# Performance work log

Hardware: AMD Instinct MI355X
Metric: run time of the kernel (lower is better)

The kernel has to match this reference:

```python
import jax, jax.numpy as jnp
import numpy as np


def setup_inputs() -> dict:
    key = jax.random.key(0)
    ks = jax.random.split(key, 6)
    B, N, D, E, S, H = 4, 4096, 768, 4, 1024, 3072
    sc = lambda d: 1.0 / np.sqrt(d)
    return {
        "x": jax.random.normal(ks[0], (B, N, D), dtype=jnp.float32),
        "phi": jax.random.normal(ks[1], (E, S, D), dtype=jnp.float32) * sc(D),
        "w1": jax.random.normal(ks[2], (E, D, H), dtype=jnp.float32) * sc(D),
        "b1": jnp.zeros((E, H), dtype=jnp.float32),
        "w2": jax.random.normal(ks[3], (E, H, D), dtype=jnp.float32) * sc(H),
        "b2": jnp.zeros((E, D), dtype=jnp.float32),
    }


def reference(x, phi, w1, b1, w2, b2):
    # x: [B,N,D], phi: [E,S,D]
    logits = jnp.einsum('bnd,esd->bnes', x, phi)          # [B,N,E,S]
    B, N, E, S = logits.shape
    dispatch = jax.nn.softmax(logits, axis=1)             # softmax over tokens
    combine = jax.nn.softmax(
        logits.reshape(B, N, E * S), axis=-1
    ).reshape(B, N, E, S)                                 # softmax over all slots
    slots = jnp.einsum('bnd,bnes->besd', x, dispatch)     # [B,E,S,D]
    h = jax.nn.gelu(jnp.einsum('besd,edh->besh', slots, w1) + b1[None, :, None, :])
    y = jnp.einsum('besh,ehd->besd', h, w2) + b2[None, :, None, :]
    out = jnp.einsum('besd,bnes->bnd', y, combine)        # [B,N,D]
    return out
```

## Files before the change

kernel.cpp:

```cpp
#include <hip/hip_runtime.h>
#include <hip/hip_bf16.h>

using u16 = unsigned short;
using short8 = __attribute__((ext_vector_type(8))) short;
using floatx4 = __attribute__((ext_vector_type(4))) float;

#define DEVI static __device__ __forceinline__

constexpr int cB = 4, cN = 4096, cD = 768, cE = 4, cS = 1024, cH = 3072;
constexpr int cES = cE * cS;

DEVI u16 f2bf(float f) {
  union { float f; unsigned u; } v; v.f = f;
  unsigned r = v.u + 0x7fffu + ((v.u >> 16) & 1u);
  return (u16)(r >> 16);
}
DEVI float bf2f(u16 b) {
  union { unsigned u; float f; } v; v.u = ((unsigned)b) << 16;
  return v.f;
}
DEVI float gelu_tanh(float x) {
  float z = 1.5957691216057308f * (x + 0.044715f * x * x * x);
  z = fminf(fmaxf(z, -30.f), 30.f);
  float e = __expf(z);
  float t = (e - 1.f) / (e + 1.f);
  return 0.5f * x * (1.f + t);
}

DEVI void glds16(const u16* g, u16* l) {
  __builtin_amdgcn_global_load_lds(
      (const __attribute__((address_space(1))) void*)g,
      (__attribute__((address_space(3))) void*)l, 16, 0, 0);
}

__global__ __launch_bounds__(256) void zero_kernel(float* __restrict__ p, int n) {
  int i = blockIdx.x * 256 + threadIdx.x;
  if (i < n) p[i] = 0.f;
}

__global__ __launch_bounds__(256) void convert_kernel(const float* __restrict__ in,
                                                      u16* __restrict__ out, long n) {
  long stride = (long)gridDim.x * 256 * 4;
  for (long idx = ((long)blockIdx.x * 256 + threadIdx.x) * 4; idx < n; idx += stride) {
    float4 v = *(const float4*)(in + idx);
    ushort4 o;
    o.x = f2bf(v.x); o.y = f2bf(v.y); o.z = f2bf(v.z); o.w = f2bf(v.w);
    *(ushort4*)(out + idx) = o;
  }
}

template <typename Tin>
__global__ __launch_bounds__(256) void transpose_bf16_kernel(const Tin* __restrict__ in,
                                                             u16* __restrict__ out,
                                                             int R, int C,
                                                             long strideIn, long strideOut) {
  __shared__ u16 tile[64][66];
  const Tin* inb = in + (long)blockIdx.z * strideIn;
  u16* outb = out + (long)blockIdx.z * strideOut;
  const int r0 = blockIdx.y * 64, c0 = blockIdx.x * 64;
  const int tid = threadIdx.x;
#pragma unroll
  for (int i = 0; i < 4; i++) {
    int v = i * 256 + tid;
    int r = v >> 4, c4 = (v & 15) * 4;
    if constexpr (sizeof(Tin) == 4) {
      float4 f = *(const float4*)&inb[(long)(r0 + r) * C + (c0 + c4)];
      tile[r][c4 + 0] = f2bf(f.x); tile[r][c4 + 1] = f2bf(f.y);
      tile[r][c4 + 2] = f2bf(f.z); tile[r][c4 + 3] = f2bf(f.w);
    } else {
      ushort4 u = *(const ushort4*)&inb[(long)(r0 + r) * C + (c0 + c4)];
      tile[r][c4 + 0] = u.x; tile[r][c4 + 1] = u.y;
      tile[r][c4 + 2] = u.z; tile[r][c4 + 3] = u.w;
    }
  }
  __syncthreads();
#pragma unroll
  for (int i = 0; i < 4; i++) {
    int w = i * 256 + tid;
    int orow = w >> 4, oc4 = (w & 15) * 4;
    ushort4 u;
    u.x = tile[oc4 + 0][orow]; u.y = tile[oc4 + 1][orow];
    u.z = tile[oc4 + 2][orow]; u.w = tile[oc4 + 3][orow];
    *(ushort4*)&outb[(long)(c0 + orow) * R + (r0 + oc4)] = u;
  }
}

template <int EPI>
__global__ __launch_bounds__(256, 2) void gemm_nt(const u16* __restrict__ A,
                                                  const u16* __restrict__ Bm,
                                                  void* __restrict__ Cout,
                                                  int M, int Nn, int K,
                                                  long ldA, long ldB, long ldC,
                                                  long strideA, long strideB, int modB,
                                                  long strideC,
                                                  const float* __restrict__ epiVec,
                                                  long epiStride, int epiMod) {
  __shared__ u16 lds[4 * 8192];

  const int gx = gridDim.x;
  const int nwg = gx * gridDim.y;
  int flat = blockIdx.y * gx + blockIdx.x;
  if ((nwg & 7) == 0) flat = (flat & 7) * (nwg >> 3) + (flat >> 3);
  const int bxs = flat % gx, bys = flat / gx;

  const int bz = blockIdx.z;
  const u16* Ab = A + (long)bz * strideA;
  const u16* Bb = Bm + (long)(bz % modB) * strideB;
  const float* ev = epiVec + (long)(bz % epiMod) * epiStride;
  const int tileM = bys * 128, tileN = bxs * 128;
  const int tid = threadIdx.x;
  const int wave = tid >> 6, lane = tid & 63;
  const int quad = lane >> 4, l16 = lane & 15;
  const int wm = (wave >> 1) * 64, wn = (wave & 1) * 64;

  const int swzk = (((lane & 3) ^ ((lane >> 3) & 3)) << 3);
  const int r0 = wave * 32 + (lane >> 2);
  const u16* aG0 = Ab + (long)(tileM + r0) * ldA + swzk;
  const u16* aG1 = Ab + (long)(tileM + r0 + 16) * ldA + swzk;
  const u16* bG0 = Bb + (long)(tileN + r0) * ldB + swzk;
  const u16* bG1 = Bb + (long)(tileN + r0 + 16) * ldB + swzk;
  const int ldsW = wave * 1024;

  const int NT = K >> 5;

  auto STAGE = [&](int tt) {
    u16* l = &lds[(tt & 3) * 8192];
    const long ko = (long)tt << 5;
    glds16(aG0 + ko, l + ldsW);
    glds16(aG1 + ko, l + ldsW + 512);
    glds16(bG0 + ko, l + 4096 + ldsW);
    glds16(bG1 + ko, l + 4096 + ldsW + 512);
  };

  floatx4 acc[4][4] = {};
  const int sread = ((quad ^ ((l16 >> 1) & 3)) << 3);

  STAGE(0);
  if (NT > 1) STAGE(1);
  if (NT > 2) STAGE(2);

  for (int t = 0; t < NT; t++) {
    asm volatile("s_barrier" ::: "memory");
    if (t + 3 < NT) STAGE(t + 3);
    const int ahead = NT - 1 - t;
    if (ahead >= 3)      asm volatile("s_waitcnt vmcnt(12)" ::: "memory");
    else if (ahead == 2) asm volatile("s_waitcnt vmcnt(8)" ::: "memory");
    else if (ahead == 1) asm volatile("s_waitcnt vmcnt(4)" ::: "memory");
    else                 asm volatile("s_waitcnt vmcnt(0)" ::: "memory");
    asm volatile("s_barrier" ::: "memory");

    const u16* As = &lds[(t & 3) * 8192];
    const u16* Bs = As + 4096;
    short8 af[4], bq[4];
#pragma unroll
    for (int i = 0; i < 4; i++)
      af[i] = *(const short8*)&As[(wm + i * 16 + l16) * 32 + sread];
#pragma unroll
    for (int j = 0; j < 4; j++)
      bq[j] = *(const short8*)&Bs[(wn + j * 16 + l16) * 32 + sread];
    __builtin_amdgcn_s_setprio(1);
#pragma unroll
    for (int i = 0; i < 4; i++)
#pragma unroll
      for (int j = 0; j < 4; j++)
        acc[i][j] = __builtin_amdgcn_mfma_f32_16x16x32_bf16(af[i], bq[j], acc[i][j], 0, 0, 0);
    __builtin_amdgcn_s_setprio(0);
  }

  const long cBase = (long)bz * strideC;
#pragma unroll
  for (int i = 0; i < 4; i++) {
#pragma unroll
    for (int r = 0; r < 4; r++) {
      const int row = tileM + wm + i * 16 + quad * 4 + r;
      float rscale = 1.f;
      if (EPI == 1 || EPI == 4) rscale = 1.f / ev[row];
#pragma unroll
      for (int j = 0; j < 4; j++) {
        const int col = tileN + wn + j * 16 + l16;
        float v = acc[i][j][r];
        const long cIdx = cBase + (long)row * ldC + col;
        if (EPI == 0) v = __expf(v);
        if (EPI == 1 || EPI == 4) v *= rscale;
        if (EPI == 2) v = gelu_tanh(v + ev[col]);
        if (EPI == 3) v = v + ev[col];
        if (EPI == 5) v = v + bf2f(((u16*)Cout)[cIdx]);
        if (EPI == 4)
          ((float*)Cout)[cIdx] = v;
        else
          ((u16*)Cout)[cIdx] = f2bf(v);
      }
    }
  }
}

template <int EPI>
__global__ __launch_bounds__(512, 2) void gemm256(const u16* __restrict__ A,
                                                  const u16* __restrict__ Bm,
                                                  void* __restrict__ Cout,
                                                  int M, int Nn, int K,
                                                  long ldA, long ldB, long ldC,
                                                  long strideA, long strideB, int modB,
                                                  long strideC,
                                                  const float* __restrict__ epiVec,
                                                  long epiStride, int epiMod,
                                                  float* __restrict__ Zc,
                                                  float* __restrict__ Zr) {
  __shared__ u16 lds[2][2][2][8192];

  const int gx = gridDim.x;
  const int nwg = gx * gridDim.y;
  int flat = blockIdx.y * gx + blockIdx.x;
  {
    const int q = nwg >> 3, r = nwg & 7, xc = flat & 7, o = flat >> 3;
    flat = (xc < r ? xc * (q + 1) : r * (q + 1) + (xc - r) * q) + o;
  }
  const int bxs = flat % gx, bys = flat / gx;

  const int bz = blockIdx.z;
  const u16* __restrict__ Ab = A + (long)bz * strideA;
  const u16* __restrict__ Bb = Bm + (long)(bz % modB) * strideB;
  const float* __restrict__ ev = epiVec + (long)(bz % epiMod) * epiStride;
  const int tileM = bys * 256, tileN = bxs * 256;
  const int tid = threadIdx.x;
  const int wave = tid >> 6, lane = tid & 63;
  const int quad = lane >> 4, l16 = lane & 15;
  const int wr = wave >> 2, wc = wave & 3;

  const int kswz = (((lane & 3) ^ ((lane >> 3) & 3)) << 3);
  const int srow = wave * 32 + (lane >> 2);
  const u16* gA = Ab + (long)(tileM + srow) * ldA + kswz;
  const u16* gB = Bb + (long)(tileN + srow) * ldB + kswz;

  const int rdsw = ((quad ^ ((l16 >> 1) & 3)) << 3);
  const int aOff = (wr * 128 + l16) * 32 + rdsw;
  const int bOff = (wc * 64 + l16) * 32 + rdsw;

  const int NT = K >> 6;

#define STA256(buf, kh, tt) do {                                   \
    const u16* _g = gA + ((long)(tt) << 6) + ((kh) << 5);          \
    u16* _l = &lds[buf][0][kh][wave * 1024];                       \
    glds16(_g, _l); glds16(_g + 16 * ldA, _l + 512); } while (0)
#define STB256(buf, kh, tt) do {                                   \
    const u16* _g = gB + ((long)(tt) << 6) + ((kh) << 5);          \
    u16* _l = &lds[buf][1][kh][wave * 1024];                       \
    glds16(_g, _l); glds16(_g + 16 * ldB, _l + 512); } while (0)
#define BAR256 asm volatile("s_barrier" ::: "memory")
#define LGK0   asm volatile("s_waitcnt lgkmcnt(0)" ::: "memory")

  floatx4 acc[8][4] = {};
  short8 af[4], bq[4];

  STA256(0, 0, 0); STB256(0, 0, 0); STA256(0, 1, 0); STB256(0, 1, 0);
  STB256(1, 0, 1); STA256(1, 0, 1); STB256(1, 1, 1);
  asm volatile("s_waitcnt vmcnt(6)" ::: "memory");
  BAR256;

#define TILE256(kt, buf) do {                                                      \
    const bool s1 = (kt) + 1 < NT, s2 = (kt) + 2 < NT;                             \
                                            \
    _Pragma("unroll") for (int i = 0; i < 4; i++)                                  \
      af[i] = *(const short8*)&lds[buf][0][0][aOff + i * 512];                     \
    _Pragma("unroll") for (int n = 0; n < 4; n++)                                  \
      bq[n] = *(const short8*)&lds[buf][1][0][bOff + n * 512];                     \
    if (s1) STA256((buf) ^ 1, 1, (kt) + 1);                                        \
    BAR256; LGK0;                                                                  \
    __builtin_amdgcn_s_setprio(1);                                                 \
    _Pragma("unroll") for (int i = 0; i < 4; i++)                                  \
      _Pragma("unroll") for (int n = 0; n < 4; n++)                                \
        acc[i][n] = __builtin_amdgcn_mfma_f32_16x16x32_bf16(af[i], bq[n], acc[i][n], 0, 0, 0); \
    __builtin_amdgcn_s_setprio(0);                                                 \
    BAR256;                                                                        \
                                         \
    _Pragma("unroll") for (int i = 0; i < 4; i++)                                  \
      af[i] = *(const short8*)&lds[buf][0][0][aOff + (4 + i) * 512];               \
    if (s2) STB256(buf, 0, (kt) + 2);                                              \
    BAR256; LGK0;                                                                  \
    __builtin_amdgcn_s_setprio(1);                                                 \
    _Pragma("unroll") for (int i = 0; i < 4; i++)                                  \
      _Pragma("unroll") for (int n = 0; n < 4; n++)                                \
        acc[4 + i][n] = __builtin_amdgcn_mfma_f32_16x16x32_bf16(af[i], bq[n], acc[4 + i][n], 0, 0, 0); \
    __builtin_amdgcn_s_setprio(0);                                                 \
    BAR256;                                                                        \
                                            \
    _Pragma("unroll") for (int i = 0; i < 4; i++)                                  \
      af[i] = *(const short8*)&lds[buf][0][1][aOff + i * 512];                     \
    _Pragma("unroll") for (int n = 0; n < 4; n++)                                  \
      bq[n] = *(const short8*)&lds[buf][1][1][bOff + n * 512];                     \
    if (s2) STA256(buf, 0, (kt) + 2);                                              \
    BAR256; LGK0;                                                                  \
    __builtin_amdgcn_s_setprio(1);                                                 \
    _Pragma("unroll") for (int i = 0; i < 4; i++)                                  \
      _Pragma("unroll") for (int n = 0; n < 4; n++)                                \
        acc[i][n] = __builtin_amdgcn_mfma_f32_16x16x32_bf16(af[i], bq[n], acc[i][n], 0, 0, 0); \
    __builtin_amdgcn_s_setprio(0);                                                 \
    BAR256;                                                                        \
                                                    \
    _Pragma("unroll") for (int i = 0; i < 4; i++)                                  \
      af[i] = *(const short8*)&lds[buf][0][1][aOff + (4 + i) * 512];               \
    if (s2) STB256(buf, 1, (kt) + 2);                                              \
    BAR256; LGK0;                                                                  \
    __builtin_amdgcn_s_setprio(1);                                                 \
    _Pragma("unroll") for (int i = 0; i < 4; i++)                                  \
      _Pragma("unroll") for (int n = 0; n < 4; n++)                                \
        acc[4 + i][n] = __builtin_amdgcn_mfma_f32_16x16x32_bf16(af[i], bq[n], acc[4 + i][n], 0, 0, 0); \
    __builtin_amdgcn_s_setprio(0);                                                 \
    if (s2)      asm volatile("s_waitcnt vmcnt(6)" ::: "memory");                  \
    else if (s1) asm volatile("s_waitcnt vmcnt(0)" ::: "memory");                  \
    BAR256;                                                                        \
  } while (0)

  for (int kt = 0; kt < NT; kt += 2) {
    TILE256(kt, 0);
    TILE256(kt + 1, 1);
  }
#undef TILE256
#undef STA256
#undef STB256
#undef BAR256
#undef LGK0

  const long cBase = (long)bz * strideC;
  if (EPI == 6) {
    float csum[4] = {0.f, 0.f, 0.f, 0.f};
#pragma unroll
    for (int m = 0; m < 8; m++) {
#pragma unroll
      for (int r = 0; r < 4; r++) {
        const int row = tileM + wr * 128 + m * 16 + quad * 4 + r;
        float rs = 0.f;
#pragma unroll
        for (int n = 0; n < 4; n++) {
          const int col = tileN + wc * 64 + n * 16 + l16;
          float v = __expf(acc[m][n][r]);
          ((u16*)Cout)[cBase + (long)row * ldC + col] = f2bf(v);
          rs += v;
          csum[n] += v;
        }
        rs += __shfl_xor(rs, 1, 64);
        rs += __shfl_xor(rs, 2, 64);
        rs += __shfl_xor(rs, 4, 64);
        rs += __shfl_xor(rs, 8, 64);
        if (l16 == 0) atomicAdd(&Zr[row], rs);
      }
    }
#pragma unroll
    for (int n = 0; n < 4; n++) {
      float c = csum[n];
      c += __shfl_xor(c, 16, 64);
      c += __shfl_xor(c, 32, 64);
      if (quad == 0) atomicAdd(&Zc[tileN + wc * 64 + n * 16 + l16], c);
    }
  } else {
#pragma unroll
    for (int m = 0; m < 8; m++) {
#pragma unroll
      for (int r = 0; r < 4; r++) {
        const int row = tileM + wr * 128 + m * 16 + quad * 4 + r;
        float rscale = 1.f;
        if (EPI == 1 || EPI == 4) rscale = 1.f / ev[row];
#pragma unroll
        for (int n = 0; n < 4; n++) {
          const int col = tileN + wc * 64 + n * 16 + l16;
          float v = acc[m][n][r];
          const long cIdx = cBase + (long)row * ldC + col;
          if (EPI == 0) v = __expf(v);
          if (EPI == 1 || EPI == 4) v *= rscale;
          if (EPI == 2) v = gelu_tanh(v + ev[col]);
          if (EPI == 3) v = v + ev[col];
          if (EPI == 5) v = v + bf2f(((u16*)Cout)[cIdx]);
          if (EPI == 4)
            ((float*)Cout)[cIdx] = v;
          else
            ((u16*)Cout)[cIdx] = f2bf(v);
        }
      }
    }
  }
}

extern "C" void kernel_launch(void* const* d_in, const int* in_sizes, int n_in,
                              void* d_out, int out_size, void* d_ws, size_t ws_size,
                              hipStream_t stream) {
  const float* x   = (const float*)d_in[0];
  const float* phi = (const float*)d_in[1];
  const float* w1  = (const float*)d_in[2];
  const float* b1  = (const float*)d_in[3];
  const float* w2  = (const float*)d_in[4];
  const float* b2  = (const float*)d_in[5];
  (void)in_sizes; (void)n_in; (void)out_size;
  float* out_f = (float*)d_out;

  char* ws = (char*)d_ws;
  size_t off = 0;
  auto carve = [&](size_t bytes) -> char* {
    char* p = ws + off;
    off += (bytes + 255) & ~(size_t)255;
    return p;
  };

  const size_t SZ_P = (size_t)cN * cES * 2;

  int nChunk = 2;
  bool cacheP = false;
  if (ws_size >= (size_t)279200000)      { cacheP = true; nChunk = 2; }
  else if (ws_size >= (size_t)262400000) { cacheP = true; nChunk = 4; }
  const int cHCx = cH / nChunk;

  u16 *Pall = nullptr, *PtA = nullptr;
  u16 *Pb = nullptr, *Ptb = nullptr, *P2 = nullptr;
  u16 *Hc, *Xbf, *Xt, *Yv, *Slots, *Yt, *Phibf, *W1t, *W2t;
  float *Z1, *Z2;

  if (cacheP) {
    Pall = (u16*)carve(4 * SZ_P);
    const size_t hcBytes = (size_t)cB * cE * cS * cHCx * 2;
    char* RS = carve(SZ_P > hcBytes ? SZ_P : hcBytes);
    PtA = (u16*)RS; Hc = (u16*)RS;
    char* XW2 = carve((size_t)cB * cN * cD * 2);
    Xbf = (u16*)XW2; W2t = (u16*)XW2;
    char* R3r = carve((size_t)cB * cD * cN * 2);
    Xt = (u16*)R3r; Yv = (u16*)R3r;
    char* R4r = carve((size_t)cB * cES * cD * 2);
    Slots = (u16*)R4r; Yt = (u16*)R4r;
    char* PW1 = carve((size_t)cE * cH * cD * 2);
    Phibf = (u16*)PW1; W1t = (u16*)PW1;
  } else {
    char* R1 = carve(2 * SZ_P);
    Pb = (u16*)R1; Ptb = (u16*)(R1 + SZ_P); Hc = (u16*)R1; P2 = (u16*)R1;
    Xbf = (u16*)carve((size_t)cB * cN * cD * 2);
    char* R3r = carve((size_t)cB * cD * cN * 2);
    Xt = (u16*)R3r; Yv = (u16*)R3r;
    char* R4r = carve((size_t)cB * cES * cD * 2);
    Slots = (u16*)R4r; Yt = (u16*)R4r;
    Phibf = (u16*)carve((size_t)cES * cD * 2);
    W1t = (u16*)carve((size_t)cE * cH * cD * 2);
    W2t = (u16*)carve((size_t)cE * cD * cH * 2);
  }
  Z1 = (float*)carve((size_t)(cB * cES + cB * cN) * 4);
  Z2 = Z1 + (size_t)cB * cES;

  convert_kernel<<<2048, 256, 0, stream>>>(x, Xbf, (long)cB * cN * cD);
  convert_kernel<<<1024, 256, 0, stream>>>(phi, Phibf, (long)cES * cD);
  transpose_bf16_kernel<float><<<dim3(cD / 64, cN / 64, cB), 256, 0, stream>>>(
      x, Xt, cN, cD, (long)cN * cD, (long)cD * cN);
  if (!cacheP) {
    transpose_bf16_kernel<float><<<dim3(cH / 64, cD / 64, cE), 256, 0, stream>>>(
        w1, W1t, cD, cH, (long)cD * cH, (long)cH * cD);
    transpose_bf16_kernel<float><<<dim3(cD / 64, cH / 64, cE), 256, 0, stream>>>(
        w2, W2t, cH, cD, (long)cH * cD, (long)cD * cH);
  }
  zero_kernel<<<(cB * (cES + cN)) / 256, 256, 0, stream>>>(Z1, cB * (cES + cN));

  for (int b = 0; b < cB; b++) {
    const u16* Xb = Xbf + (long)b * cN * cD;
    u16* Pdst = cacheP ? Pall + (size_t)b * cN * cES : Pb;
    u16* Ptmp = cacheP ? PtA : Ptb;
    gemm256<6><<<dim3(cES / 256, cN / 256, 1), 512, 0, stream>>>(
        Xb, Phibf, Pdst, cN, cES, cD, cD, cD, cES,
        0L, 0L, 1, 0L, Z1, 0, 1,
        Z1 + (long)b * cES, Z2 + (long)b * cN);
    transpose_bf16_kernel<u16><<<dim3(cES / 64, cN / 64, 1), 256, 0, stream>>>(
        Pdst, Ptmp, cN, cES, 0L, 0L);
    gemm_nt<1><<<dim3(cD / 128, cES / 128, 1), 256, 0, stream>>>(
        Ptmp, Xt + (long)b * cD * cN, Slots + (long)b * cES * cD,
        cES, cD, cN, cN, cN, cD,
        0L, 0L, 1, 0L, Z1 + (long)b * cES, 0, 1);
  }

  if (cacheP) {
    transpose_bf16_kernel<float><<<dim3(cH / 64, cD / 64, cE), 256, 0, stream>>>(
        w1, W1t, cD, cH, (long)cD * cH, (long)cH * cD);
    transpose_bf16_kernel<float><<<dim3(cD / 64, cH / 64, cE), 256, 0, stream>>>(
        w2, W2t, cH, cD, (long)cH * cD, (long)cD * cH);
  }

  for (int hc = 0; hc < nChunk; hc++) {
    const int h0 = hc * cHCx;
    gemm256<2><<<dim3(cHCx / 256, cS / 256, cB * cE), 512, 0, stream>>>(
        Slots, W1t + (long)h0 * cD, Hc, cS, cHCx, cD, cD, cD, cHCx,
        (long)cS * cD, (long)cH * cD, cE, (long)cS * cHCx, b1 + h0, cH, cE,
        nullptr, nullptr);
    if (hc == 0)
      gemm256<3><<<dim3(cD / 256, cS / 256, cB * cE), 512, 0, stream>>>(
          Hc, W2t + h0, Yv, cS, cD, cHCx, cHCx, cH, cD,
          (long)cS * cHCx, (long)cD * cH, cE, (long)cS * cD, b2, cD, cE,
          nullptr, nullptr);
    else
      gemm256<5><<<dim3(cD / 256, cS / 256, cB * cE), 512, 0, stream>>>(
          Hc, W2t + h0, Yv, cS, cD, cHCx, cHCx, cH, cD,
          (long)cS * cHCx, (long)cD * cH, cE, (long)cS * cD, b2, cD, cE,
          nullptr, nullptr);
  }

  transpose_bf16_kernel<u16><<<dim3(cD / 64, cES / 64, cB), 256, 0, stream>>>(
      Yv, Yt, cES, cD, (long)cES * cD, (long)cD * cES);
  for (int bp = 0; bp < 2; bp++) {
    const u16* Psrc;
    if (cacheP) {
      Psrc = Pall + (size_t)(bp * 2) * cN * cES;
    } else {
      const u16* Xb = Xbf + (long)(bp * 2) * cN * cD;
      gemm256<0><<<dim3(cES / 256, cN / 256, 2), 512, 0, stream>>>(
          Xb, Phibf, P2, cN, cES, cD, cD, cD, cES,
          (long)cN * cD, 0L, 1, (long)cN * cES, Z1, 0, 1, nullptr, nullptr);
      Psrc = P2;
    }
    gemm_nt<4><<<dim3(cD / 128, cN / 128, 2), 256, 0, stream>>>(
        Psrc, Yt + (long)(bp * 2) * cD * cES, out_f + (long)(bp * 2) * cN * cD,
        cN, cD, cES, cES, cES, cD,
        (long)cN * cES, (long)cD * cES, 2, (long)cN * cD,
        Z2 + (long)(bp * 2) * cN, cN, 2);
  }
}
```

Before: 1.059 ms.

## Replace 256-tile GEMM with simpler 128-tile kernel and batch logits GEMM

Replaces the hand-pipelined 256x256 GEMM (512 threads, 8-stage LDS schedule) with a simpler 128x128 tile kernel using 256 threads, K-step 32 and plain double buffering. The logits GEMM for all batches now runs as one batched launch when P is cached. W2 is transposed per H-chunk into a smaller buffer, and the cached path now uses three chunks. Smaller tiles give more workgroups and occupancy but less data reuse per tile and more barriers per K.

```diff
diff --git a/kernel.cpp b/kernel.cpp
--- a/kernel.cpp
+++ b/kernel.cpp
@@ -195,18 +195,20 @@
 }
 
 template <int EPI>
-__global__ __launch_bounds__(512, 2) void gemm256(const u16* __restrict__ A,
-                                                  const u16* __restrict__ Bm,
-                                                  void* __restrict__ Cout,
-                                                  int M, int Nn, int K,
-                                                  long ldA, long ldB, long ldC,
-                                                  long strideA, long strideB, int modB,
-                                                  long strideC,
-                                                  const float* __restrict__ epiVec,
-                                                  long epiStride, int epiMod,
-                                                  float* __restrict__ Zc,
-                                                  float* __restrict__ Zr) {
-  __shared__ u16 lds[2][2][2][8192];
+__global__ __launch_bounds__(256, 4) void gemm_s(const u16* __restrict__ A,
+                                                 const u16* __restrict__ Bm,
+                                                 void* __restrict__ Cout,
+                                                 int M, int Nn, int K,
+                                                 long ldA, long ldB, long ldC,
+                                                 long strideA, long strideB, int modB,
+                                                 long strideC,
+                                                 const float* __restrict__ epiVec,
+                                                 long epiStride, int epiMod,
+                                                 float* __restrict__ Zc,
+                                                 float* __restrict__ Zr,
+                                                 long zcs, long zrs) {
+  __shared__ u16 As[2][4096];
+  __shared__ u16 Bs[2][4096];
 
   const int gx = gridDim.x;
   const int nwg = gx * gridDim.y;
@@ -221,149 +223,100 @@
   const u16* __restrict__ Ab = A + (long)bz * strideA;
   const u16* __restrict__ Bb = Bm + (long)(bz % modB) * strideB;
   const float* __restrict__ ev = epiVec + (long)(bz % epiMod) * epiStride;
-  const int tileM = bys * 256, tileN = bxs * 256;
+  const int tileM = bys * 128, tileN = bxs * 128;
   const int tid = threadIdx.x;
   const int wave = tid >> 6, lane = tid & 63;
   const int quad = lane >> 4, l16 = lane & 15;
-  const int wr = wave >> 2, wc = wave & 3;
+  const int wm = (wave >> 1) * 64, wn = (wave & 1) * 64;
 
   const int kswz = (((lane & 3) ^ ((lane >> 3) & 3)) << 3);
-  const int srow = wave * 32 + (lane >> 2);
-  const u16* gA = Ab + (long)(tileM + srow) * ldA + kswz;
-  const u16* gB = Bb + (long)(tileN + srow) * ldB + kswz;
-
-  const int rdsw = ((quad ^ ((l16 >> 1) & 3)) << 3);
-  const int aOff = (wr * 128 + l16) * 32 + rdsw;
-  const int bOff = (wc * 64 + l16) * 32 + rdsw;
-
-  const int NT = K >> 6;
-
-#define STA256(buf, kh, tt) do {                                   \
-    const u16* _g = gA + ((long)(tt) << 6) + ((kh) << 5);          \
-    u16* _l = &lds[buf][0][kh][wave * 1024];                       \
-    glds16(_g, _l); glds16(_g + 16 * ldA, _l + 512); } while (0)
-#define STB256(buf, kh, tt) do {                                   \
-    const u16* _g = gB + ((long)(tt) << 6) + ((kh) << 5);          \
-    u16* _l = &lds[buf][1][kh][wave * 1024];                       \
-    glds16(_g, _l); glds16(_g + 16 * ldB, _l + 512); } while (0)
-#define BAR256 asm volatile("s_barrier" ::: "memory")
-#define LGK0   asm volatile("s_waitcnt lgkmcnt(0)" ::: "memory")
-
-  floatx4 acc[8][4] = {};
-  short8 af[4], bq[4];
-
-  STA256(0, 0, 0); STB256(0, 0, 0); STA256(0, 1, 0); STB256(0, 1, 0);
-  STB256(1, 0, 1); STA256(1, 0, 1); STB256(1, 1, 1);
-  asm volatile("s_waitcnt vmcnt(6)" ::: "memory");
-  BAR256;
-
-#define TILE256(kt, buf) do {                                                      \
-    const bool s1 = (kt) + 1 < NT, s2 = (kt) + 2 < NT;                             \
-                                            \
-    _Pragma("unroll") for (int i = 0; i < 4; i++)                                  \
-      af[i] = *(const short8*)&lds[buf][0][0][aOff + i * 512];                     \
-    _Pragma("unroll") for (int n = 0; n < 4; n++)                                  \
-      bq[n] = *(const short8*)&lds[buf][1][0][bOff + n * 512];                     \
-    if (s1) STA256((buf) ^ 1, 1, (kt) + 1);                                        \
-    BAR256; LGK0;                                                                  \
-    __builtin_amdgcn_s_setprio(1);                                                 \
-    _Pragma("unroll") for (int i = 0; i < 4; i++)                                  \
-      _Pragma("unroll") for (int n = 0; n < 4; n++)                                \
-        acc[i][n] = __builtin_amdgcn_mfma_f32_16x16x32_bf16(af[i], bq[n], acc[i][n], 0, 0, 0); \
-    __builtin_amdgcn_s_setprio(0);                                                 \
-    BAR256;                                                                        \
-                                         \
-    _Pragma("unroll") for (int i = 0; i < 4; i++)                                  \
-      af[i] = *(const short8*)&lds[buf][0][0][aOff + (4 + i) * 512];               \
-    if (s2) STB256(buf, 0, (kt) + 2);                                              \
-    BAR256; LGK0;                                                                  \
-    __builtin_amdgcn_s_setprio(1);                                                 \
-    _Pragma("unroll") for (int i = 0; i < 4; i++)                                  \
-      _Pragma("unroll") for (int n = 0; n < 4; n++)                                \
-        acc[4 + i][n] = __builtin_amdgcn_mfma_f32_16x16x32_bf16(af[i], bq[n], acc[4 + i][n], 0, 0, 0); \
-    __builtin_amdgcn_s_setprio(0);                                                 \
-    BAR256;                                                                        \
-                                            \
-    _Pragma("unroll") for (int i = 0; i < 4; i++)                                  \
-      af[i] = *(const short8*)&lds[buf][0][1][aOff + i * 512];                     \
-    _Pragma("unroll") for (int n = 0; n < 4; n++)                                  \
-      bq[n] = *(const short8*)&lds[buf][1][1][bOff + n * 512];                     \
-    if (s2) STA256(buf, 0, (kt) + 2);                                              \
-    BAR256; LGK0;                                                                  \
-    __builtin_amdgcn_s_setprio(1);                                                 \
-    _Pragma("unroll") for (int i = 0; i < 4; i++)                                  \
-      _Pragma("unroll") for (int n = 0; n < 4; n++)                                \
-        acc[i][n] = __builtin_amdgcn_mfma_f32_16x16x32_bf16(af[i], bq[n], acc[i][n], 0, 0, 0); \
-    __builtin_amdgcn_s_setprio(0);                                                 \
-    BAR256;                                                                        \
-                                                    \
-    _Pragma("unroll") for (int i = 0; i < 4; i++)                                  \
-      af[i] = *(const short8*)&lds[buf][0][1][aOff + (4 + i) * 512];               \
-    if (s2) STB256(buf, 1, (kt) + 2);                                              \
-    BAR256; LGK0;                                                                  \
-    __builtin_amdgcn_s_setprio(1);                                                 \
-    _Pragma("unroll") for (int i = 0; i < 4; i++)                                  \
-      _Pragma("unroll") for (int n = 0; n < 4; n++)                                \
-        acc[4 + i][n] = __builtin_amdgcn_mfma_f32_16x16x32_bf16(af[i], bq[n], acc[4 + i][n], 0, 0, 0); \
-    __builtin_amdgcn_s_setprio(0);                                                 \
-    if (s2)      asm volatile("s_waitcnt vmcnt(6)" ::: "memory");                  \
-    else if (s1) asm volatile("s_waitcnt vmcnt(0)" ::: "memory");                  \
-    BAR256;                                                                        \
-  } while (0)
-
-  for (int kt = 0; kt < NT; kt += 2) {
-    TILE256(kt, 0);
-    TILE256(kt + 1, 1);
-  }
-#undef TILE256
-#undef STA256
-#undef STB256
-#undef BAR256
-#undef LGK0
+  const int r0 = wave * 32 + (lane >> 2);
+  const u16* aG0 = Ab + (long)(tileM + r0) * ldA + kswz;
+  const u16* aG1 = Ab + (long)(tileM + r0 + 16) * ldA + kswz;
+  const u16* bG0 = Bb + (long)(tileN + r0) * ldB + kswz;
+  const u16* bG1 = Bb + (long)(tileN + r0 + 16) * ldB + kswz;
+  const int ldsW = wave * 1024;
+
+  const int NT = K >> 5;
+  floatx4 acc[4][4] = {};
+  const int sread = ((quad ^ ((l16 >> 1) & 3)) << 3);
+
+  auto STAGE = [&](int tt) {
+    const int bf = tt & 1;
+    const long ko = (long)tt << 5;
+    glds16(aG0 + ko, &As[bf][ldsW]);
+    glds16(aG1 + ko, &As[bf][ldsW + 512]);
+    glds16(bG0 + ko, &Bs[bf][ldsW]);
+    glds16(bG1 + ko, &Bs[bf][ldsW + 512]);
+  };
+
+  STAGE(0);
+  for (int t = 0; t < NT; t++) {
+    __syncthreads();
+    if (t + 1 < NT) STAGE(t + 1);
+    const u16* Ap = As[t & 1];
+    const u16* Bp = Bs[t & 1];
+    short8 af[4], bq[4];
+#pragma unroll
+    for (int i = 0; i < 4; i++)
+      af[i] = *(const short8*)&Ap[(wm + i * 16 + l16) * 32 + sread];
+#pragma unroll
+    for (int j = 0; j < 4; j++)
+      bq[j] = *(const short8*)&Bp[(wn + j * 16 + l16) * 32 + sread];
+    __builtin_amdgcn_s_setprio(1);
+#pragma unroll
+    for (int i = 0; i < 4; i++)
+#pragma unroll
+      for (int j = 0; j < 4; j++)
+        acc[i][j] = __builtin_amdgcn_mfma_f32_16x16x32_bf16(af[i], bq[j], acc[i][j], 0, 0, 0);
+    __builtin_amdgcn_s_setprio(0);
+  }
 
   const long cBase = (long)bz * strideC;
   if (EPI == 6) {
+    float* zc = Zc + (long)bz * zcs;
+    float* zr = Zr + (long)bz * zrs;
     float csum[4] = {0.f, 0.f, 0.f, 0.f};
 #pragma unroll
-    for (int m = 0; m < 8; m++) {
+    for (int i = 0; i < 4; i++) {
 #pragma unroll
       for (int r = 0; r < 4; r++) {
-        const int row = tileM + wr * 128 + m * 16 + quad * 4 + r;
+        const int row = tileM + wm + i * 16 + quad * 4 + r;
         float rs = 0.f;
 #pragma unroll
-        for (int n = 0; n < 4; n++) {
-          const int col = tileN + wc * 64 + n * 16 + l16;
-          float v = __expf(acc[m][n][r]);
+        for (int j = 0; j < 4; j++) {
+          const int col = tileN + wn + j * 16 + l16;
+          float v = __expf(acc[i][j][r]);
           ((u16*)Cout)[cBase + (long)row * ldC + col] = f2bf(v);
           rs += v;
-          csum[n] += v;
+          csum[j] += v;
         }
         rs += __shfl_xor(rs, 1, 64);
         rs += __shfl_xor(rs, 2, 64);
         rs += __shfl_xor(rs, 4, 64);
         rs += __shfl_xor(rs, 8, 64);
-        if (l16 == 0) atomicAdd(&Zr[row], rs);
+        if (l16 == 0) atomicAdd(&zr[row], rs);
       }
     }
 #pragma unroll
-    for (int n = 0; n < 4; n++) {
-      float c = csum[n];
+    for (int j = 0; j < 4; j++) {
+      float c = csum[j];
       c += __shfl_xor(c, 16, 64);
       c += __shfl_xor(c, 32, 64);
-      if (quad == 0) atomicAdd(&Zc[tileN + wc * 64 + n * 16 + l16], c);
+      if (quad == 0) atomicAdd(&zc[tileN + wn + j * 16 + l16], c);
     }
   } else {
 #pragma unroll
-    for (int m = 0; m < 8; m++) {
+    for (int i = 0; i < 4; i++) {
 #pragma unroll
       for (int r = 0; r < 4; r++) {
-        const int row = tileM + wr * 128 + m * 16 + quad * 4 + r;
+        const int row = tileM + wm + i * 16 + quad * 4 + r;
         float rscale = 1.f;
         if (EPI == 1 || EPI == 4) rscale = 1.f / ev[row];
 #pragma unroll
-        for (int n = 0; n < 4; n++) {
-          const int col = tileN + wc * 64 + n * 16 + l16;
-          float v = acc[m][n][r];
+        for (int j = 0; j < 4; j++) {
+          const int col = tileN + wn + j * 16 + l16;
+          float v = acc[i][j][r];
           const long cIdx = cBase + (long)row * ldC + col;
           if (EPI == 0) v = __expf(v);
           if (EPI == 1 || EPI == 4) v *= rscale;
@@ -402,30 +355,27 @@
 
   const size_t SZ_P = (size_t)cN * cES * 2;
 
-  int nChunk = 2;
-  bool cacheP = false;
-  if (ws_size >= (size_t)279200000)      { cacheP = true; nChunk = 2; }
-  else if (ws_size >= (size_t)262400000) { cacheP = true; nChunk = 4; }
+  const bool cacheP = ws_size >= (size_t)262400000;
+  const int nChunk = cacheP ? 3 : 2;
   const int cHCx = cH / nChunk;
 
-  u16 *Pall = nullptr, *PtA = nullptr;
+  u16 *Pall = nullptr, *PtA = nullptr, *W2c = nullptr;
   u16 *Pb = nullptr, *Ptb = nullptr, *P2 = nullptr;
-  u16 *Hc, *Xbf, *Xt, *Yv, *Slots, *Yt, *Phibf, *W1t, *W2t;
+  u16 *Hc, *Xbf, *Xt, *Yv, *Slots, *Yt, *Phibf, *W1t, *W2t = nullptr;
   float *Z1, *Z2;
 
   if (cacheP) {
     Pall = (u16*)carve(4 * SZ_P);
-    const size_t hcBytes = (size_t)cB * cE * cS * cHCx * 2;
-    char* RS = carve(SZ_P > hcBytes ? SZ_P : hcBytes);
+    char* RS = carve(SZ_P);
     PtA = (u16*)RS; Hc = (u16*)RS;
-    char* XW2 = carve((size_t)cB * cN * cD * 2);
-    Xbf = (u16*)XW2; W2t = (u16*)XW2;
-    char* R3r = carve((size_t)cB * cD * cN * 2);
-    Xt = (u16*)R3r; Yv = (u16*)R3r;
-    char* R4r = carve((size_t)cB * cES * cD * 2);
-    Slots = (u16*)R4r; Yt = (u16*)R4r;
-    char* PW1 = carve((size_t)cE * cH * cD * 2);
-    Phibf = (u16*)PW1; W1t = (u16*)PW1;
+    char* RX = carve((size_t)cB * cN * cD * 2);
+    Xbf = (u16*)RX; W2c = (u16*)RX;
+    char* RY = carve((size_t)cB * cD * cN * 2);
+    Xt = (u16*)RY; Yv = (u16*)RY;
+    char* RZ = carve((size_t)cB * cES * cD * 2);
+    Slots = (u16*)RZ; Yt = (u16*)RZ;
+    char* RW = carve((size_t)cE * cH * cD * 2);
+    Phibf = (u16*)RW; W1t = (u16*)RW;
   } else {
     char* R1 = carve(2 * SZ_P);
     Pb = (u16*)R1; Ptb = (u16*)(R1 + SZ_P); Hc = (u16*)R1; P2 = (u16*)R1;
@@ -453,45 +403,62 @@
   }
   zero_kernel<<<(cB * (cES + cN)) / 256, 256, 0, stream>>>(Z1, cB * (cES + cN));
 
-  for (int b = 0; b < cB; b++) {
-    const u16* Xb = Xbf + (long)b * cN * cD;
-    u16* Pdst = cacheP ? Pall + (size_t)b * cN * cES : Pb;
-    u16* Ptmp = cacheP ? PtA : Ptb;
-    gemm256<6><<<dim3(cES / 256, cN / 256, 1), 512, 0, stream>>>(
-        Xb, Phibf, Pdst, cN, cES, cD, cD, cD, cES,
-        0L, 0L, 1, 0L, Z1, 0, 1,
-        Z1 + (long)b * cES, Z2 + (long)b * cN);
-    transpose_bf16_kernel<u16><<<dim3(cES / 64, cN / 64, 1), 256, 0, stream>>>(
-        Pdst, Ptmp, cN, cES, 0L, 0L);
-    gemm_nt<1><<<dim3(cD / 128, cES / 128, 1), 256, 0, stream>>>(
-        Ptmp, Xt + (long)b * cD * cN, Slots + (long)b * cES * cD,
-        cES, cD, cN, cN, cN, cD,
-        0L, 0L, 1, 0L, Z1 + (long)b * cES, 0, 1);
-  }
-
   if (cacheP) {
+    gemm_s<6><<<dim3(cES / 128, cN / 128, cB), 256, 0, stream>>>(
+        Xbf, Phibf, Pall, cN, cES, cD, cD, cD, cES,
+        (long)cN * cD, 0L, 1, (long)cN * cES, Z1, 0, 1,
+        Z1, Z2, (long)cES, (long)cN);
+    for (int b = 0; b < cB; b++) {
+      transpose_bf16_kernel<u16><<<dim3(cES / 64, cN / 64, 1), 256, 0, stream>>>(
+          Pall + (size_t)b * cN * cES, PtA, cN, cES, 0L, 0L);
+      gemm_nt<1><<<dim3(cD / 128, cES / 128, 1), 256, 0, stream>>>(
+          PtA, Xt + (long)b * cD * cN, Slots + (long)b * cES * cD,
+          cES, cD, cN, cN, cN, cD,
+          0L, 0L, 1, 0L, Z1 + (long)b * cES, 0, 1);
+    }
     transpose_bf16_kernel<float><<<dim3(cH / 64, cD / 64, cE), 256, 0, stream>>>(
         w1, W1t, cD, cH, (long)cD * cH, (long)cH * cD);
-    transpose_bf16_kernel<float><<<dim3(cD / 64, cH / 64, cE), 256, 0, stream>>>(
-        w2, W2t, cH, cD, (long)cH * cD, (long)cD * cH);
+  } else {
+    for (int b = 0; b < cB; b++) {
+      const u16* Xb = Xbf + (long)b * cN * cD;
+      gemm_s<6><<<dim3(cES / 128, cN / 128, 1), 256, 0, stream>>>(
+          Xb, Phibf, Pb, cN, cES, cD, cD, cD, cES,
+          0L, 0L, 1, 0L, Z1, 0, 1,
+          Z1 + (long)b * cES, Z2 + (long)b * cN, 0L, 0L);
+      transpose_bf16_kernel<u16><<<dim3(cES / 64, cN / 64, 1), 256, 0, stream>>>(
+          Pb, Ptb, cN, cES, 0L, 0L);
+      gemm_nt<1><<<dim3(cD / 128, cES / 128, 1), 256, 0, stream>>>(
+          Ptb, Xt + (long)b * cD * cN, Slots + (long)b * cES * cD,
+          cES, cD, cN, cN, cN, cD,
+          0L, 0L, 1, 0L, Z1 + (long)b * cES, 0, 1);
+    }
   }
 
   for (int hc = 0; hc < nChunk; hc++) {
     const int h0 = hc * cHCx;
-    gemm256<2><<<dim3(cHCx / 256, cS / 256, cB * cE), 512, 0, stream>>>(
+    const u16* W2base;
+    long ldB2, strideB2;
+    if (cacheP) {
+      transpose_bf16_kernel<float><<<dim3(cD / 64, cHCx / 64, cE), 256, 0, stream>>>(
+          w2 + (long)h0 * cD, W2c, cHCx, cD, (long)cH * cD, (long)cD * cHCx);
+      W2base = W2c; ldB2 = cHCx; strideB2 = (long)cD * cHCx;
+    } else {
+      W2base = W2t + h0; ldB2 = cH; strideB2 = (long)cD * cH;
+    }
+    gemm_s<2><<<dim3(cHCx / 128, cS / 128, cB * cE), 256, 0, stream>>>(
         Slots, W1t + (long)h0 * cD, Hc, cS, cHCx, cD, cD, cD, cHCx,
         (long)cS * cD, (long)cH * cD, cE, (long)cS * cHCx, b1 + h0, cH, cE,
-        nullptr, nullptr);
+        nullptr, nullptr, 0L, 0L);
     if (hc == 0)
-      gemm256<3><<<dim3(cD / 256, cS / 256, cB * cE), 512, 0, stream>>>(
-          Hc, W2t + h0, Yv, cS, cD, cHCx, cHCx, cH, cD,
-          (long)cS * cHCx, (long)cD * cH, cE, (long)cS * cD, b2, cD, cE,
-          nullptr, nullptr);
+      gemm_s<3><<<dim3(cD / 128, cS / 128, cB * cE), 256, 0, stream>>>(
+          Hc, W2base, Yv, cS, cD, cHCx, cHCx, ldB2, cD,
+          (long)cS * cHCx, strideB2, cE, (long)cS * cD, b2, cD, cE,
+          nullptr, nullptr, 0L, 0L);
     else
-      gemm256<5><<<dim3(cD / 256, cS / 256, cB * cE), 512, 0, stream>>>(
-          Hc, W2t + h0, Yv, cS, cD, cHCx, cHCx, cH, cD,
-          (long)cS * cHCx, (long)cD * cH, cE, (long)cS * cD, b2, cD, cE,
-          nullptr, nullptr);
+      gemm_s<5><<<dim3(cD / 128, cS / 128, cB * cE), 256, 0, stream>>>(
+          Hc, W2base, Yv, cS, cD, cHCx, cHCx, ldB2, cD,
+          (long)cS * cHCx, strideB2, cE, (long)cS * cD, b2, cD, cE,
+          nullptr, nullptr, 0L, 0L);
   }
 
   transpose_bf16_kernel<u16><<<dim3(cD / 64, cES / 64, cB), 256, 0, stream>>>(
@@ -502,9 +469,10 @@
       Psrc = Pall + (size_t)(bp * 2) * cN * cES;
     } else {
       const u16* Xb = Xbf + (long)(bp * 2) * cN * cD;
-      gemm256<0><<<dim3(cES / 256, cN / 256, 2), 512, 0, stream>>>(
+      gemm_s<0><<<dim3(cES / 128, cN / 128, 2), 256, 0, stream>>>(
           Xb, Phibf, P2, cN, cES, cD, cD, cD, cES,
-          (long)cN * cD, 0L, 1, (long)cN * cES, Z1, 0, 1, nullptr, nullptr);
+          (long)cN * cD, 0L, 1, (long)cN * cES, Z1, 0, 1,
+          nullptr, nullptr, 0L, 0L);
       Psrc = P2;
     }
     gemm_nt<4><<<dim3(cD / 128, cN / 128, 2), 256, 0, stream>>>(
```

Measured after the change: 1.020 ms. 1.04x faster.
